# Kernel tuning notes

Hardware: AMD Instinct MI355X
Metric: run time of the kernel (lower is better)

Reference implementation:

```python
import jax, jax.numpy as jnp
import numpy as np

DMODEL = 512
NUM_HEADS = 8
HEAD_DIM = DMODEL // NUM_HEADS


def setup_inputs() -> dict:
    key = jax.random.key(0)
    k1, k2, k3, k4, k5 = jax.random.split(key, 5)
    x = jax.random.normal(k1, (4, 2048, DMODEL), dtype=jnp.float32)
    s = 1.0 / np.sqrt(DMODEL)
    W_qkv = jax.random.uniform(k2, (DMODEL, 3 * DMODEL), jnp.float32, -s, s)
    b_qkv = jax.random.uniform(k3, (3 * DMODEL,), jnp.float32, -s, s)
    W_out = jax.random.uniform(k4, (DMODEL, DMODEL), jnp.float32, -s, s)
    b_out = jax.random.uniform(k5, (DMODEL,), jnp.float32, -s, s)
    return {"x": x, "W_qkv": W_qkv, "b_qkv": b_qkv, "W_out": W_out, "b_out": b_out}


def reference(x, W_qkv, b_qkv, W_out, b_out):
    B, T, D = x.shape
    H, Hd = NUM_HEADS, HEAD_DIM
    qkv = x @ W_qkv + b_qkv                      # [B, T, 3D]
    qkv = qkv.reshape(B, T, 3, H, Hd).transpose(2, 0, 3, 1, 4)  # [3, B, H, T, Hd]
    q, k, v = qkv[0], qkv[1], qkv[2]
    scores = jnp.einsum('bhqd,bhkd->bhqk', q, k) / np.sqrt(Hd)  # [B, H, T, T]
    causal = jnp.tril(jnp.ones((T, T), dtype=bool))
    scores = jnp.where(causal, scores, -jnp.inf)
    weights = jax.nn.softmax(scores, axis=-1)
    out = jnp.einsum('bhqk,bhkd->bhqd', weights, v)  # [B, H, T, Hd]
    out = out.transpose(0, 2, 1, 3).reshape(B, T, D)
    return out @ W_out + b_out
```

## Files before the change

### kernel.cpp

```cpp
#include <hip/hip_runtime.h>
#include <cstdint>
#include <cstddef>

#define D_MODEL 512
#define SEQ_T 2048
#define NHEADS 8
#define HDIM 64

typedef __attribute__((ext_vector_type(8))) short bf16x8;
typedef __attribute__((ext_vector_type(4))) float f32x4;
typedef __attribute__((ext_vector_type(16))) float f32x16;
typedef __attribute__((ext_vector_type(2))) unsigned int uint2v;

__device__ __forceinline__ unsigned short f2bf(float f) {
  unsigned int u = __float_as_uint(f);
  u += 0x7FFFu + ((u >> 16) & 1u);
  return (unsigned short)(u >> 16);
}

__device__ __forceinline__ unsigned int pack_bf16(float lo, float hi) {
  unsigned int a = __float_as_uint(lo) + 0x8000u;
  unsigned int b = __float_as_uint(hi) + 0x8000u;
  return __builtin_amdgcn_perm(b, a, 0x07060302u);
}

__device__ __forceinline__ void plswap(unsigned int& a, unsigned int& b) {
  uint2v r = __builtin_amdgcn_permlane32_swap(a, b, false, false);
  a = r[0];
  b = r[1];
}

#define QSCALE 0.18033688011112043f
#define SSHIFT 16.0f

__device__ __forceinline__ void async_lds16(const unsigned short* g,
                                            unsigned short* l) {
  __builtin_amdgcn_global_load_lds(
      (const __attribute__((address_space(1))) void*)g,
      (__attribute__((address_space(3))) void*)l, 16, 0, 0);
}

__global__ __launch_bounds__(256) void prep_kernel(
    const float* __restrict__ x, const float* __restrict__ W_qkv,
    const float* __restrict__ W_out, unsigned short* __restrict__ xb,
    unsigned short* __restrict__ Wqkt, unsigned short* __restrict__ Wot) {
  __shared__ float tile[64][65];
  const int bid = blockIdx.x;
  if (bid < 2048) {
    int i = (bid * 256 + threadIdx.x) * 8;
    float4 a = *(const float4*)(x + i);
    float4 b = *(const float4*)(x + i + 4);
    ushort4 lo = {f2bf(a.x), f2bf(a.y), f2bf(a.z), f2bf(a.w)};
    ushort4 hi = {f2bf(b.x), f2bf(b.y), f2bf(b.z), f2bf(b.w)};
    *(ushort4*)(xb + i) = lo;
    *(ushort4*)(xb + i + 4) = hi;
    return;
  }
  const float* src;
  unsigned short* dst;
  int R = 512, C, c0, r0;
  if (bid < 2048 + 192) {
    int t = bid - 2048;
    C = 1536; c0 = (t % 24) * 64; r0 = (t / 24) * 64;
    src = W_qkv; dst = Wqkt;
  } else {
    int t = bid - 2240;
    C = 512; c0 = (t & 7) * 64; r0 = (t >> 3) * 64;
    src = W_out; dst = Wot;
  }
  for (int i = threadIdx.x; i < 64 * 64; i += 256) {
    int r = i >> 6, c = i & 63;
    tile[r][c] = src[(size_t)(r0 + r) * C + c0 + c];
  }
  __syncthreads();
  for (int i = threadIdx.x; i < 64 * 64; i += 256) {
    int c = i >> 6, r = i & 63;
    dst[(size_t)(c0 + c) * R + r0 + r] = f2bf(tile[r][c]);
  }
}

__global__ __launch_bounds__(256) void gemm_qkv_mfma(
    const unsigned short* __restrict__ xb, const unsigned short* __restrict__ Wt,
    const float* __restrict__ bias, unsigned short* __restrict__ Qtb,
    unsigned short* __restrict__ Kb, unsigned short* __restrict__ Vtb) {
  __shared__ unsigned short As[128 * 64];
  __shared__ unsigned short Bs[128 * 64];
  const int tid = threadIdx.x;
  const int w = tid >> 6, lane = tid & 63;
  const int quad = lane >> 4, l15 = lane & 15;
  const int wm = w >> 1, wn = w & 1;
  const int m0 = blockIdx.x * 128, n0 = blockIdx.y * 128;

  const int srow = tid >> 3;
  const int schunk = (tid & 7) ^ (srow & 7);
  const unsigned short* ga = xb + (size_t)(m0 + srow) * 512 + schunk * 8;
  const unsigned short* gb = Wt + (size_t)(n0 + srow) * 512 + schunk * 8;
  unsigned short* lA = As + tid * 8;
  unsigned short* lB = Bs + tid * 8;

  f32x4 acc[4][4] = {};
  for (int k0 = 0; k0 < 512; k0 += 64) {
#pragma unroll
    for (int rr = 0; rr < 4; ++rr) {
      async_lds16(ga + (size_t)rr * 32 * 512 + k0, lA + rr * 2048);
      async_lds16(gb + (size_t)rr * 32 * 512 + k0, lB + rr * 2048);
    }
    __syncthreads();
    bf16x8 af[4][2], bfr[4][2];
#pragma unroll
    for (int mb = 0; mb < 4; ++mb) {
      int row = wm * 64 + mb * 16 + l15;
#pragma unroll
      for (int kk = 0; kk < 2; ++kk) {
        int slot = (kk * 4 + quad) ^ (row & 7);
        af[mb][kk] = *(const bf16x8*)&As[row * 64 + slot * 8];
      }
    }
#pragma unroll
    for (int nb = 0; nb < 4; ++nb) {
      int row = wn * 64 + nb * 16 + l15;
#pragma unroll
      for (int kk = 0; kk < 2; ++kk) {
        int slot = (kk * 4 + quad) ^ (row & 7);
        bfr[nb][kk] = *(const bf16x8*)&Bs[row * 64 + slot * 8];
      }
    }
#pragma unroll
    for (int mb = 0; mb < 4; ++mb)
#pragma unroll
      for (int nb = 0; nb < 4; ++nb) {
        acc[mb][nb] = __builtin_amdgcn_mfma_f32_16x16x32_bf16(
            af[mb][0], bfr[nb][0], acc[mb][nb], 0, 0, 0);
        acc[mb][nb] = __builtin_amdgcn_mfma_f32_16x16x32_bf16(
            af[mb][1], bfr[nb][1], acc[mb][nb], 0, 0, 0);
      }
    __syncthreads();
  }

  const int cbase = n0 + wn * 64;
  const int three = cbase >> 9;
  const int h = (cbase >> 6) & 7;
  const int bh = ((m0 >> 11) << 3) + h;
  const int t0 = (m0 & 2047) + wm * 64;
  float bv[4];
#pragma unroll
  for (int nb = 0; nb < 4; ++nb) bv[nb] = bias[cbase + nb * 16 + l15];

  if (three == 0) {
#pragma unroll
    for (int mb = 0; mb < 4; ++mb)
#pragma unroll
      for (int nb = 0; nb < 4; ++nb) {
        int trow = t0 + mb * 16 + quad * 4;
        ushort4 v = {f2bf((acc[mb][nb][0] + bv[nb]) * QSCALE),
                     f2bf((acc[mb][nb][1] + bv[nb]) * QSCALE),
                     f2bf((acc[mb][nb][2] + bv[nb]) * QSCALE),
                     f2bf((acc[mb][nb][3] + bv[nb]) * QSCALE)};
        *(ushort4*)(Qtb + ((size_t)bh * HDIM + nb * 16 + l15) * SEQ_T + trow) = v;
      }
  } else if (three == 2) {
#pragma unroll
    for (int mb = 0; mb < 4; ++mb)
#pragma unroll
      for (int nb = 0; nb < 4; ++nb) {
        int trow = t0 + mb * 16 + quad * 4;
        ushort4 v = {f2bf(acc[mb][nb][0] + bv[nb]), f2bf(acc[mb][nb][1] + bv[nb]),
                     f2bf(acc[mb][nb][2] + bv[nb]), f2bf(acc[mb][nb][3] + bv[nb])};
        *(ushort4*)(Vtb + ((size_t)bh * HDIM + nb * 16 + l15) * SEQ_T + trow) = v;
      }
  } else {
#pragma unroll
    for (int mb = 0; mb < 4; ++mb)
#pragma unroll
      for (int nb = 0; nb < 4; ++nb)
#pragma unroll
        for (int r = 0; r < 4; ++r) {
          int trow = t0 + mb * 16 + quad * 4 + r;
          Kb[((size_t)bh * SEQ_T + trow) * HDIM + nb * 16 + l15] =
              f2bf(acc[mb][nb][r] + bv[nb]);
        }
  }
}

__global__ __launch_bounds__(256, 2) void attn_mfma7(
    const unsigned short* __restrict__ Qtb, const unsigned short* __restrict__ Kb,
    const unsigned short* __restrict__ Vtb, unsigned short* __restrict__ AOb) {
  __shared__ __align__(16) unsigned short Ks[2][64 * 64];
  __shared__ __align__(16) unsigned short Vs[2][64 * 64];
  const int tid = threadIdx.x;
  const int w = tid >> 6, lane = tid & 63;
  const int l31 = lane & 31, h = lane >> 5;
  const int r7l = lane & 7;

  const int bid = blockIdx.x;
  const int xcd = bid & 7;
  const int j = bid >> 3;
  const int c = j & 31, g = j >> 5;
  const int kslot = c >> 2;
  const int bh = xcd + 8 * (c & 3);
  const int qt2 = g ? kslot : (15 - kslot);
  const int nmain = 2 * qt2;

  const unsigned short* kbase = Kb + (size_t)bh * SEQ_T * HDIM;
  const unsigned short* vbase = Vtb + (size_t)bh * HDIM * SEQ_T;
  const int sr = tid >> 3;
  const int lc = tid & 7;
  const int sw8 = (lc ^ (sr & 7)) * 8;

  auto stage = [&](int b, int kt) {
    const unsigned short* kp = kbase + (size_t)(kt * 64 + sr) * 64 + sw8;
    async_lds16(kp, &Ks[b][tid * 8]);
    async_lds16(kp + 32 * 64, &Ks[b][2048 + tid * 8]);
    const unsigned short* vp = vbase + (size_t)sr * SEQ_T + kt * 64 + sw8;
    async_lds16(vp, &Vs[b][tid * 8]);
    async_lds16(vp + (size_t)32 * SEQ_T, &Vs[b][2048 + tid * 8]);
  };

  const int qglob = qt2 * 128 + w * 32 + l31;
  bf16x8 qf[4];
  {
    unsigned short qraw[32];
    const unsigned short* qp =
        Qtb + ((size_t)bh * HDIM + h * 8) * SEQ_T + qglob;
#pragma unroll
    for (int cc = 0; cc < 4; ++cc)
#pragma unroll
      for (int jj = 0; jj < 8; ++jj)
        qraw[cc * 8 + jj] = qp[(size_t)(cc * 16 + jj) * SEQ_T];
#pragma unroll
    for (int cc = 0; cc < 4; ++cc) qf[cc] = *(const bf16x8*)(qraw + cc * 8);
  }

  f32x16 O0 = {0.f, 0.f, 0.f, 0.f, 0.f, 0.f, 0.f, 0.f,
               0.f, 0.f, 0.f, 0.f, 0.f, 0.f, 0.f, 0.f};
  f32x16 O1 = O0;
  float l_acc = 0.f;

  auto tile_compute = [&](int cur, int lim, bool masked) {
    f32x16 S0 = {0.f, 0.f, 0.f, 0.f, 0.f, 0.f, 0.f, 0.f,
                 0.f, 0.f, 0.f, 0.f, 0.f, 0.f, 0.f, 0.f};
    f32x16 S1 = S0;
    __builtin_amdgcn_s_setprio(1);
#pragma unroll
    for (int cc = 0; cc < 4; ++cc) {
      const int slot = ((cc << 1) | h) ^ r7l;
      const bf16x8 k0 = *(const bf16x8*)&Ks[cur][l31 * 64 + slot * 8];
      const bf16x8 k1 = *(const bf16x8*)&Ks[cur][(32 + l31) * 64 + slot * 8];
      S0 = __builtin_amdgcn_mfma_f32_32x32x16_bf16(k0, qf[cc], S0, 0, 0, 0);
      S1 = __builtin_amdgcn_mfma_f32_32x32x16_bf16(k1, qf[cc], S1, 0, 0, 0);
    }
    __builtin_amdgcn_s_setprio(0);
    unsigned int pk0[8], pk1[8];
#pragma unroll
    for (int m = 0; m < 8; ++m) {
      float p0 = __builtin_amdgcn_exp2f(S0[2 * m] - SSHIFT);
      float p1 = __builtin_amdgcn_exp2f(S0[2 * m + 1] - SSHIFT);
      float p2 = __builtin_amdgcn_exp2f(S1[2 * m] - SSHIFT);
      float p3 = __builtin_amdgcn_exp2f(S1[2 * m + 1] - SSHIFT);
      if (masked) {
        const int r0 = 2 * m, r1 = 2 * m + 1;
        const int kl0 = (r0 & 3) + 8 * (r0 >> 2) + 4 * h;
        const int kl1 = (r1 & 3) + 8 * (r1 >> 2) + 4 * h;
        p0 = (kl0 > lim) ? 0.f : p0;
        p1 = (kl1 > lim) ? 0.f : p1;
        p2 = (kl0 + 32 > lim) ? 0.f : p2;
        p3 = (kl1 + 32 > lim) ? 0.f : p3;
      }
      l_acc += (p0 + p1) + (p2 + p3);
      pk0[m] = pack_bf16(p0, p1);
      pk1[m] = pack_bf16(p2, p3);
    }
#pragma unroll
    for (int tp = 0; tp < 2; ++tp) {
      plswap(pk0[4 * tp + 0], pk0[4 * tp + 2]);
      plswap(pk0[4 * tp + 1], pk0[4 * tp + 3]);
      plswap(pk1[4 * tp + 0], pk1[4 * tp + 2]);
      plswap(pk1[4 * tp + 1], pk1[4 * tp + 3]);
    }
#pragma unroll
    for (int kb = 0; kb < 2; ++kb)
#pragma unroll
      for (int tp = 0; tp < 2; ++tp) {
        const int t = 2 * kb + tp;
        uint4 wv;
        if (kb == 0)
          wv = (uint4){pk0[4 * tp + 0], pk0[4 * tp + 1], pk0[4 * tp + 2],
                       pk0[4 * tp + 3]};
        else
          wv = (uint4){pk1[4 * tp + 0], pk1[4 * tp + 1], pk1[4 * tp + 2],
                       pk1[4 * tp + 3]};
        const bf16x8 pb = *(const bf16x8*)&wv;
        const int slot = ((t << 1) | h) ^ r7l;
        const bf16x8 v0 = *(const bf16x8*)&Vs[cur][l31 * 64 + slot * 8];
        const bf16x8 v1 = *(const bf16x8*)&Vs[cur][(32 + l31) * 64 + slot * 8];
        __builtin_amdgcn_s_setprio(1);
        O0 = __builtin_amdgcn_mfma_f32_32x32x16_bf16(v0, pb, O0, 0, 0, 0);
        O1 = __builtin_amdgcn_mfma_f32_32x32x16_bf16(v1, pb, O1, 0, 0, 0);
        __builtin_amdgcn_s_setprio(0);
      }
  };

  stage(0, 0);
  __syncthreads();

  for (int i = 0; i < nmain; ++i) {
    const int cur = i & 1;
    stage(cur ^ 1, i + 1);
    tile_compute(cur, 0, false);
    __syncthreads();
  }

  {
    const int cur = nmain & 1;
    stage(cur ^ 1, nmain + 1);
    tile_compute(cur, w * 32 + l31, true);
    __syncthreads();
  }

  if (w >= 2) {
    const int cur = (nmain + 1) & 1;
    tile_compute(cur, w * 32 + l31 - 64, true);
  }

  l_acc += __shfl_xor(l_acc, 32, 64);
  const float inv = 1.0f / fmaxf(l_acc, 1e-30f);
  const int bb = bh >> 3, hh = bh & 7;
  unsigned short* dst = AOb + ((size_t)bb * SEQ_T + qglob) * D_MODEL + (hh << 6);
#pragma unroll
  for (int rg = 0; rg < 4; ++rg) {
    ushort4 o0 = {f2bf(O0[4 * rg + 0] * inv), f2bf(O0[4 * rg + 1] * inv),
                  f2bf(O0[4 * rg + 2] * inv), f2bf(O0[4 * rg + 3] * inv)};
    *(ushort4*)(dst + 8 * rg + 4 * h) = o0;
    ushort4 o1 = {f2bf(O1[4 * rg + 0] * inv), f2bf(O1[4 * rg + 1] * inv),
                  f2bf(O1[4 * rg + 2] * inv), f2bf(O1[4 * rg + 3] * inv)};
    *(ushort4*)(dst + 32 + 8 * rg + 4 * h) = o1;
  }
}

__global__ __launch_bounds__(256) void gemm_out_mfma(
    const unsigned short* __restrict__ AOb, const unsigned short* __restrict__ Wot,
    const float* __restrict__ bias, float* __restrict__ out) {
  __shared__ unsigned short As[64 * 64];
  __shared__ unsigned short Bs[128 * 64];
  const int tid = threadIdx.x;
  const int w = tid >> 6, lane = tid & 63;
  const int quad = lane >> 4, l15 = lane & 15;
  const int m0 = blockIdx.x * 64, n0 = blockIdx.y * 128;

  const int srow = tid >> 3;
  const int schunk = (tid & 7) ^ (srow & 7);
  const unsigned short* ga = AOb + (size_t)(m0 + srow) * 512 + schunk * 8;
  const unsigned short* gb = Wot + (size_t)(n0 + srow) * 512 + schunk * 8;
  unsigned short* lA = As + tid * 8;
  unsigned short* lB = Bs + tid * 8;

  f32x4 acc[4][2] = {};
  for (int k0 = 0; k0 < 512; k0 += 64) {
#pragma unroll
    for (int rr = 0; rr < 2; ++rr)
      async_lds16(ga + (size_t)rr * 32 * 512 + k0, lA + rr * 2048);
#pragma unroll
    for (int rr = 0; rr < 4; ++rr)
      async_lds16(gb + (size_t)rr * 32 * 512 + k0, lB + rr * 2048);
    __syncthreads();
    bf16x8 af[4][2], bfr[2][2];
#pragma unroll
    for (int mb = 0; mb < 4; ++mb) {
      int row = mb * 16 + l15;
#pragma unroll
      for (int kk = 0; kk < 2; ++kk) {
        int slot = (kk * 4 + quad) ^ (row & 7);
        af[mb][kk] = *(const bf16x8*)&As[row * 64 + slot * 8];
      }
    }
#pragma unroll
    for (int nb = 0; nb < 2; ++nb) {
      int row = w * 32 + nb * 16 + l15;
#pragma unroll
      for (int kk = 0; kk < 2; ++kk) {
        int slot = (kk * 4 + quad) ^ (row & 7);
        bfr[nb][kk] = *(const bf16x8*)&Bs[row * 64 + slot * 8];
      }
    }
#pragma unroll
    for (int mb = 0; mb < 4; ++mb)
#pragma unroll
      for (int nb = 0; nb < 2; ++nb) {
        acc[mb][nb] = __builtin_amdgcn_mfma_f32_16x16x32_bf16(
            af[mb][0], bfr[nb][0], acc[mb][nb], 0, 0, 0);
        acc[mb][nb] = __builtin_amdgcn_mfma_f32_16x16x32_bf16(
            af[mb][1], bfr[nb][1], acc[mb][nb], 0, 0, 0);
      }
    __syncthreads();
  }

  const int cbase = n0 + w * 32;
  float bv[2];
#pragma unroll
  for (int nb = 0; nb < 2; ++nb) bv[nb] = bias[cbase + nb * 16 + l15];
#pragma unroll
  for (int mb = 0; mb < 4; ++mb)
#pragma unroll
    for (int nb = 0; nb < 2; ++nb)
#pragma unroll
      for (int r = 0; r < 4; ++r)
        out[(size_t)(m0 + mb * 16 + quad * 4 + r) * 512 + cbase + nb * 16 +
            l15] = acc[mb][nb][r] + bv[nb];
}

extern "C" void kernel_launch(void* const* d_in, const int* in_sizes, int n_in,
                              void* d_out, int out_size, void* d_ws,
                              size_t ws_size, hipStream_t stream) {
  const float* x     = (const float*)d_in[0];
  const float* W_qkv = (const float*)d_in[1];
  const float* b_qkv = (const float*)d_in[2];
  const float* W_out = (const float*)d_in[3];
  const float* b_out = (const float*)d_in[4];
  float* out = (float*)d_out;

  const size_t NX = (size_t)4 * SEQ_T * D_MODEL;
  unsigned short* xb   = (unsigned short*)d_ws;
  unsigned short* Wqkt = xb + NX;
  unsigned short* Wot  = Wqkt + (size_t)1536 * 512;
  unsigned short* Qtb  = Wot + (size_t)512 * 512;
  unsigned short* Kb   = Qtb + NX;
  unsigned short* Vtb  = Kb + NX;
  unsigned short* AOb  = Vtb + NX;

  prep_kernel<<<2304, 256, 0, stream>>>(x, W_qkv, W_out, xb, Wqkt, Wot);
  gemm_qkv_mfma<<<dim3(64, 12), 256, 0, stream>>>(xb, Wqkt, b_qkv, Qtb, Kb,
                                                  Vtb);
  attn_mfma7<<<dim3(512), 256, 0, stream>>>(Qtb, Kb, Vtb, AOb);
  gemm_out_mfma<<<dim3(128, 4), 256, 0, stream>>>(AOb, Wot, b_out, out);
}
```

Before: 147.3 us.

## Split attention KV tiles across wave pairs and pair query tiles per block

The attention kernel now gives each block two 64-row query tiles (pr and 31-pr) so every block gets a balanced amount of causal work, in place of one 128-row tile with an XCD-aware mapping. Within a block, two waves cover each 32-row query half and split the key tiles between them, even and odd. Their partial O and l sums are combined through LDS before the write-out. This is meant to even out causal load imbalance and raise the number of waves working per query row. In exchange it adds an LDS reduction with extra barriers, stages twice as much KV per step, and drops the XCD-locality block mapping.

```diff
diff --git a/kernel.cpp b/kernel.cpp
--- a/kernel.cpp
+++ b/kernel.cpp
@@ -182,24 +182,20 @@
   }
 }
 
-__global__ __launch_bounds__(256, 2) void attn_mfma7(
+__global__ __launch_bounds__(256, 2) void attn_mfma8(
     const unsigned short* __restrict__ Qtb, const unsigned short* __restrict__ Kb,
     const unsigned short* __restrict__ Vtb, unsigned short* __restrict__ AOb) {
-  __shared__ __align__(16) unsigned short Ks[2][64 * 64];
-  __shared__ __align__(16) unsigned short Vs[2][64 * 64];
+  __shared__ __align__(16) unsigned short Kp[2][2][64 * 64];
+  __shared__ __align__(16) unsigned short Vp[2][2][64 * 64];
   const int tid = threadIdx.x;
   const int w = tid >> 6, lane = tid & 63;
   const int l31 = lane & 31, h = lane >> 5;
   const int r7l = lane & 7;
+  const int qhalf = w & 1, ks = w >> 1;
 
   const int bid = blockIdx.x;
-  const int xcd = bid & 7;
-  const int j = bid >> 3;
-  const int c = j & 31, g = j >> 5;
-  const int kslot = c >> 2;
-  const int bh = xcd + 8 * (c & 3);
-  const int qt2 = g ? kslot : (15 - kslot);
-  const int nmain = 2 * qt2;
+  const int bh = bid & 31;
+  const int pr = bid >> 5;
 
   const unsigned short* kbase = Kb + (size_t)bh * SEQ_T * HDIM;
   const unsigned short* vbase = Vtb + (size_t)bh * HDIM * SEQ_T;
@@ -207,45 +203,30 @@
   const int lc = tid & 7;
   const int sw8 = (lc ^ (sr & 7)) * 8;
 
-  auto stage = [&](int b, int kt) {
+  auto stage1 = [&](int b, int p, int kt) {
     const unsigned short* kp = kbase + (size_t)(kt * 64 + sr) * 64 + sw8;
-    async_lds16(kp, &Ks[b][tid * 8]);
-    async_lds16(kp + 32 * 64, &Ks[b][2048 + tid * 8]);
+    async_lds16(kp, &Kp[b][p][tid * 8]);
+    async_lds16(kp + 32 * 64, &Kp[b][p][2048 + tid * 8]);
     const unsigned short* vp = vbase + (size_t)sr * SEQ_T + kt * 64 + sw8;
-    async_lds16(vp, &Vs[b][tid * 8]);
-    async_lds16(vp + (size_t)32 * SEQ_T, &Vs[b][2048 + tid * 8]);
+    async_lds16(vp, &Vp[b][p][tid * 8]);
+    async_lds16(vp + (size_t)32 * SEQ_T, &Vp[b][p][2048 + tid * 8]);
   };
 
-  const int qglob = qt2 * 128 + w * 32 + l31;
+  const f32x16 Z16 = {0.f, 0.f, 0.f, 0.f, 0.f, 0.f, 0.f, 0.f,
+                      0.f, 0.f, 0.f, 0.f, 0.f, 0.f, 0.f, 0.f};
+  f32x16 O0 = Z16, O1 = Z16;
+  float l_acc = 0.f;
   bf16x8 qf[4];
-  {
-    unsigned short qraw[32];
-    const unsigned short* qp =
-        Qtb + ((size_t)bh * HDIM + h * 8) * SEQ_T + qglob;
-#pragma unroll
-    for (int cc = 0; cc < 4; ++cc)
-#pragma unroll
-      for (int jj = 0; jj < 8; ++jj)
-        qraw[cc * 8 + jj] = qp[(size_t)(cc * 16 + jj) * SEQ_T];
-#pragma unroll
-    for (int cc = 0; cc < 4; ++cc) qf[cc] = *(const bf16x8*)(qraw + cc * 8);
-  }
-
-  f32x16 O0 = {0.f, 0.f, 0.f, 0.f, 0.f, 0.f, 0.f, 0.f,
-               0.f, 0.f, 0.f, 0.f, 0.f, 0.f, 0.f, 0.f};
-  f32x16 O1 = O0;
-  float l_acc = 0.f;
-
-  auto tile_compute = [&](int cur, int lim, bool masked) {
-    f32x16 S0 = {0.f, 0.f, 0.f, 0.f, 0.f, 0.f, 0.f, 0.f,
-                 0.f, 0.f, 0.f, 0.f, 0.f, 0.f, 0.f, 0.f};
-    f32x16 S1 = S0;
+
+  auto tile_compute = [&](const unsigned short* Ksrc,
+                          const unsigned short* Vsrc, int lim, bool masked) {
+    f32x16 S0 = Z16, S1 = Z16;
     __builtin_amdgcn_s_setprio(1);
 #pragma unroll
     for (int cc = 0; cc < 4; ++cc) {
       const int slot = ((cc << 1) | h) ^ r7l;
-      const bf16x8 k0 = *(const bf16x8*)&Ks[cur][l31 * 64 + slot * 8];
-      const bf16x8 k1 = *(const bf16x8*)&Ks[cur][(32 + l31) * 64 + slot * 8];
+      const bf16x8 k0 = *(const bf16x8*)&Ksrc[l31 * 64 + slot * 8];
+      const bf16x8 k1 = *(const bf16x8*)&Ksrc[(32 + l31) * 64 + slot * 8];
       S0 = __builtin_amdgcn_mfma_f32_32x32x16_bf16(k0, qf[cc], S0, 0, 0, 0);
       S1 = __builtin_amdgcn_mfma_f32_32x32x16_bf16(k1, qf[cc], S1, 0, 0, 0);
     }
@@ -291,8 +272,8 @@
                        pk1[4 * tp + 3]};
         const bf16x8 pb = *(const bf16x8*)&wv;
         const int slot = ((t << 1) | h) ^ r7l;
-        const bf16x8 v0 = *(const bf16x8*)&Vs[cur][l31 * 64 + slot * 8];
-        const bf16x8 v1 = *(const bf16x8*)&Vs[cur][(32 + l31) * 64 + slot * 8];
+        const bf16x8 v0 = *(const bf16x8*)&Vsrc[l31 * 64 + slot * 8];
+        const bf16x8 v1 = *(const bf16x8*)&Vsrc[(32 + l31) * 64 + slot * 8];
         __builtin_amdgcn_s_setprio(1);
         O0 = __builtin_amdgcn_mfma_f32_32x32x16_bf16(v0, pb, O0, 0, 0, 0);
         O1 = __builtin_amdgcn_mfma_f32_32x32x16_bf16(v1, pb, O1, 0, 0, 0);
@@ -300,40 +281,83 @@
       }
   };
 
-  stage(0, 0);
-  __syncthreads();
-
-  for (int i = 0; i < nmain; ++i) {
-    const int cur = i & 1;
-    stage(cur ^ 1, i + 1);
-    tile_compute(cur, 0, false);
-    __syncthreads();
-  }
-
-  {
-    const int cur = nmain & 1;
-    stage(cur ^ 1, nmain + 1);
-    tile_compute(cur, w * 32 + l31, true);
-    __syncthreads();
-  }
-
-  if (w >= 2) {
-    const int cur = (nmain + 1) & 1;
-    tile_compute(cur, w * 32 + l31 - 64, true);
-  }
-
-  l_acc += __shfl_xor(l_acc, 32, 64);
-  const float inv = 1.0f / fmaxf(l_acc, 1e-30f);
-  const int bb = bh >> 3, hh = bh & 7;
-  unsigned short* dst = AOb + ((size_t)bb * SEQ_T + qglob) * D_MODEL + (hh << 6);
-#pragma unroll
-  for (int rg = 0; rg < 4; ++rg) {
-    ushort4 o0 = {f2bf(O0[4 * rg + 0] * inv), f2bf(O0[4 * rg + 1] * inv),
-                  f2bf(O0[4 * rg + 2] * inv), f2bf(O0[4 * rg + 3] * inv)};
-    *(ushort4*)(dst + 8 * rg + 4 * h) = o0;
-    ushort4 o1 = {f2bf(O1[4 * rg + 0] * inv), f2bf(O1[4 * rg + 1] * inv),
-                  f2bf(O1[4 * rg + 2] * inv), f2bf(O1[4 * rg + 3] * inv)};
-    *(ushort4*)(dst + 32 + 8 * rg + 4 * h) = o1;
+  for (int ph = 0; ph < 2; ++ph) {
+    const int qt = ph ? (31 - pr) : pr;
+    const int qglob = qt * 64 + qhalf * 32 + l31;
+
+    {
+      unsigned short qraw[32];
+      const unsigned short* qp =
+          Qtb + ((size_t)bh * HDIM + h * 8) * SEQ_T + qglob;
+#pragma unroll
+      for (int cc = 0; cc < 4; ++cc)
+#pragma unroll
+        for (int jj = 0; jj < 8; ++jj)
+          qraw[cc * 8 + jj] = qp[(size_t)(cc * 16 + jj) * SEQ_T];
+#pragma unroll
+      for (int cc = 0; cc < 4; ++cc) qf[cc] = *(const bf16x8*)(qraw + cc * 8);
+    }
+    O0 = Z16;
+    O1 = Z16;
+    l_acc = 0.f;
+
+    const int S = (qt + 2) >> 1;
+    stage1(0, 0, 0);
+    stage1(0, 1, qt < 1 ? qt : 1);
+    __syncthreads();
+
+    for (int s = 0; s < S; ++s) {
+      const int cur = s & 1;
+      if (s + 1 < S) {
+        const int ka = 2 * s + 2, kb2 = 2 * s + 3;
+        stage1(cur ^ 1, 0, ka > qt ? qt : ka);
+        stage1(cur ^ 1, 1, kb2 > qt ? qt : kb2);
+      }
+      const int kt = 2 * s + ks;
+      if (kt <= qt) {
+        if (kt == qt)
+          tile_compute(&Kp[cur][ks][0], &Vp[cur][ks][0], qhalf * 32 + l31,
+                       true);
+        else
+          tile_compute(&Kp[cur][ks][0], &Vp[cur][ks][0], 0, false);
+      }
+      __syncthreads();
+    }
+
+    l_acc += __shfl_xor(l_acc, 32, 64);
+    float* osc = (float*)&Kp[0][0][0];
+    float* lsc = (float*)&Vp[0][0][0];
+    if (ks == 1) {
+#pragma unroll
+      for (int r = 0; r < 16; ++r) {
+        osc[(qhalf * 32 + r) * 64 + lane] = O0[r];
+        osc[(qhalf * 32 + 16 + r) * 64 + lane] = O1[r];
+      }
+      lsc[qhalf * 64 + lane] = l_acc;
+    }
+    __syncthreads();
+    if (ks == 0) {
+      l_acc += lsc[qhalf * 64 + lane];
+      const float inv = 1.0f / fmaxf(l_acc, 1e-30f);
+#pragma unroll
+      for (int r = 0; r < 16; ++r) {
+        O0[r] += osc[(qhalf * 32 + r) * 64 + lane];
+        O1[r] += osc[(qhalf * 32 + 16 + r) * 64 + lane];
+      }
+      const int bb = bh >> 3, hh = bh & 7;
+      unsigned short* dst =
+          AOb + ((size_t)bb * SEQ_T + qglob) * D_MODEL + (hh << 6);
+#pragma unroll
+      for (int rg = 0; rg < 4; ++rg) {
+        ushort4 o0 = {f2bf(O0[4 * rg + 0] * inv), f2bf(O0[4 * rg + 1] * inv),
+                      f2bf(O0[4 * rg + 2] * inv), f2bf(O0[4 * rg + 3] * inv)};
+        *(ushort4*)(dst + 8 * rg + 4 * h) = o0;
+        ushort4 o1 = {f2bf(O1[4 * rg + 0] * inv), f2bf(O1[4 * rg + 1] * inv),
+                      f2bf(O1[4 * rg + 2] * inv), f2bf(O1[4 * rg + 3] * inv)};
+        *(ushort4*)(dst + 32 + 8 * rg + 4 * h) = o1;
+      }
+    }
+    __syncthreads();
   }
 }
 
@@ -430,6 +454,6 @@
   prep_kernel<<<2304, 256, 0, stream>>>(x, W_qkv, W_out, xb, Wqkt, Wot);
   gemm_qkv_mfma<<<dim3(64, 12), 256, 0, stream>>>(xb, Wqkt, b_qkv, Qtb, Kb,
                                                   Vtb);
-  attn_mfma7<<<dim3(512), 256, 0, stream>>>(Qtb, Kb, Vtb, AOb);
+  attn_mfma8<<<dim3(512), 256, 0, stream>>>(Qtb, Kb, Vtb, AOb);
   gemm_out_mfma<<<dim3(128, 4), 256, 0, stream>>>(AOb, Wot, b_out, out);
 }
```

After: 137.8 us. 6.5% less time.
